# Performance work log

Hardware: AMD Instinct MI355X
Metric: run time of the kernel (lower is better)

## Reference

```python
import jax, jax.numpy as jnp
import numpy as np

N_HEADS = 16
D_MODEL = 1024
D_K = 64
D_V = 64
LN_EPS = 1e-6


def setup_inputs() -> dict:
    key = jax.random.key(0)
    ks = jax.random.split(key, 16)
    B, L, D = 4, 512, D_MODEL
    s = 1.0 / np.sqrt(D)
    return {
        "q": jax.random.normal(ks[0], (B, L, D), jnp.float32),
        "k": jax.random.normal(ks[1], (B, L, D), jnp.float32),
        "v": jax.random.normal(ks[2], (B, L, D), jnp.float32),
        "bias": jax.random.normal(ks[3], (B, N_HEADS, L, L), jnp.float32),
        "graph_attn_bias": jax.random.normal(ks[4], (B, N_HEADS, L, L), jnp.float32),
        # projection weights stored as [in, out] (math-equivalent to torch Linear)
        "wq": jax.random.normal(ks[5], (D, N_HEADS * D_K), jnp.float32) * s,
        "bq": jnp.zeros((N_HEADS * D_K,), jnp.float32),
        "wk": jax.random.normal(ks[6], (D, N_HEADS * D_K), jnp.float32) * s,
        "bk": jnp.zeros((N_HEADS * D_K,), jnp.float32),
        "wv": jax.random.normal(ks[7], (D, N_HEADS * D_V), jnp.float32) * s,
        "bv": jnp.zeros((N_HEADS * D_V,), jnp.float32),
        "wo": jax.random.normal(ks[8], (N_HEADS * D_V, D), jnp.float32) * s,
        "bo": jnp.zeros((D,), jnp.float32),
        "ln_g": jnp.ones((D,), jnp.float32),
        "ln_b": jnp.zeros((D,), jnp.float32),
    }


def reference(q, k, v, bias, graph_attn_bias, wq, bq, wk, bk, wv, bv, wo, bo, ln_g, ln_b):
    B, Lq, D = q.shape
    H, dk, dv = N_HEADS, D_K, D_V
    residual = q
    # fused QKV projections, split heads -> [B, H, L, d]
    qh = (q @ wq + bq).reshape(B, Lq, H, dk).transpose(0, 2, 1, 3)
    kh = (k @ wk + bk).reshape(B, k.shape[1], H, dk).transpose(0, 2, 1, 3)
    vh = (v @ wv + bv).reshape(B, v.shape[1], H, dv).transpose(0, 2, 1, 3)
    # graph scaled dot-product attention: scores + mask bias + structural bias
    scores = jnp.einsum("bhqd,bhkd->bhqk", qh / np.sqrt(dk).astype(qh.dtype), kh)
    scores = scores + bias + graph_attn_bias
    weights = jax.nn.softmax(scores, axis=-1)
    ctx = jnp.einsum("bhqk,bhkd->bhqd", weights, vh)  # [B,H,Lq,dv]
    ctx = ctx.transpose(0, 2, 1, 3).reshape(B, Lq, H * dv)
    out = ctx @ wo + bo + residual
    # LayerNorm(eps=1e-6)
    mu = jnp.mean(out, axis=-1, keepdims=True)
    var = jnp.var(out, axis=-1, keepdims=True)
    out = (out - mu) * jax.lax.rsqrt(var + LN_EPS) * ln_g + ln_b
    return out
```

## Files before the change

kernel.cpp:

```cpp
#include <hip/hip_runtime.h>

#define D_MODEL 1024
#define N_HEADS 16
#define DK 64
#define LSEQ 512
#define BATCH 4
#define M_ROWS (BATCH * LSEQ)

typedef unsigned short ushort_t;
typedef __attribute__((ext_vector_type(8))) short short8;
typedef __attribute__((ext_vector_type(4))) float floatx4;

__device__ __forceinline__ float bf2f(unsigned short u) {
    return __uint_as_float(((unsigned int)u) << 16);
}
__device__ __forceinline__ unsigned short f2bf(float f) {
    unsigned int u = __float_as_uint(f);
    u += 0x7fffu + ((u >> 16) & 1u);
    return (unsigned short)(u >> 16);
}

__global__ __launch_bounds__(256) void cast3_kernel(
    const float* __restrict__ a, const float* __restrict__ b,
    const float* __restrict__ c, ushort_t* __restrict__ oa,
    ushort_t* __restrict__ ob, ushort_t* __restrict__ oc, int n)
{
    const float* src = (blockIdx.y == 0) ? a : (blockIdx.y == 1) ? b : c;
    ushort_t* dst = (blockIdx.y == 0) ? oa : (blockIdx.y == 1) ? ob : oc;
    int i = (blockIdx.x * 256 + threadIdx.x) * 4;
    if (i + 3 < n) {
        float4 v = *(const float4*)(src + i);
        ushort4 o = make_ushort4(f2bf(v.x), f2bf(v.y), f2bf(v.z), f2bf(v.w));
        *(ushort4*)(dst + i) = o;
    }
}

__global__ __launch_bounds__(256) void transpose4_kernel(
    const float* __restrict__ w0, const float* __restrict__ w1,
    const float* __restrict__ w2, const float* __restrict__ w3,
    ushort_t* __restrict__ o0, ushort_t* __restrict__ o1,
    ushort_t* __restrict__ o2, ushort_t* __restrict__ o3)
{
    __shared__ float tile[32][33];
    const float* W = (blockIdx.z == 0) ? w0 : (blockIdx.z == 1) ? w1
                   : (blockIdx.z == 2) ? w2 : w3;
    ushort_t* O = (blockIdx.z == 0) ? o0 : (blockIdx.z == 1) ? o1
                : (blockIdx.z == 2) ? o2 : o3;
    const int tx = threadIdx.x & 31;
    const int ty = threadIdx.x >> 5;
    const int kbase = blockIdx.y * 32;
    const int nbase = blockIdx.x * 32;
    #pragma unroll
    for (int j = 0; j < 4; ++j)
        tile[ty + 8 * j][tx] = W[(size_t)(kbase + ty + 8 * j) * 1024 + nbase + tx];
    __syncthreads();
    #pragma unroll
    for (int j = 0; j < 4; ++j) {
        int n = nbase + ty + 8 * j;
        O[(size_t)n * 1024 + kbase + tx] = f2bf(tile[tx][ty + 8 * j]);
    }
}

template <bool OUT_BF16, bool ADD_RES>
__device__ __forceinline__ void gemm_bt_body(
    const ushort_t* __restrict__ A, const ushort_t* __restrict__ Bt,
    const float* __restrict__ bvec, const float* __restrict__ res,
    void* __restrict__ outp, int M, int N, int K,
    int rowBase, int colBase, ushort_t* As, ushort_t* Bs)
{
    const int tid = threadIdx.x;
    const int l = tid & 63;
    const int w = tid >> 6;
    const int wave_m = w >> 1;
    const int wave_n = w & 1;

    const int srow = l >> 2;
    const int skof = (l & 3) * 8;
    const ushort_t* gA = A  + (size_t)(rowBase + w * 16 + srow) * K + skof;
    const ushort_t* gB = Bt + (size_t)(colBase + w * 16 + srow) * K + skof;
    ushort_t* lA = As + w * 512;
    ushort_t* lB = Bs + w * 512;

    floatx4 acc[2][2];
    #pragma unroll
    for (int i = 0; i < 2; ++i)
        #pragma unroll
        for (int j = 0; j < 2; ++j)
            acc[i][j] = (floatx4){0.f, 0.f, 0.f, 0.f};

    const int fm = l & 15;
    const int fk = (l >> 4) * 8;

    for (int k0 = 0; k0 < K; k0 += 32) {
        __builtin_amdgcn_global_load_lds(
            (const __attribute__((address_space(1))) void*)(gA + k0),
            (__attribute__((address_space(3))) void*)lA, 16, 0, 0);
        __builtin_amdgcn_global_load_lds(
            (const __attribute__((address_space(1))) void*)(gB + k0),
            (__attribute__((address_space(3))) void*)lB, 16, 0, 0);
        __syncthreads();

        short8 afrag[2], bfrag[2];
        #pragma unroll
        for (int mi = 0; mi < 2; ++mi)
            afrag[mi] = *(const short8*)&As[(wave_m * 32 + mi * 16 + fm) * 32 + fk];
        #pragma unroll
        for (int ni = 0; ni < 2; ++ni)
            bfrag[ni] = *(const short8*)&Bs[(wave_n * 32 + ni * 16 + fm) * 32 + fk];

        #pragma unroll
        for (int mi = 0; mi < 2; ++mi)
            #pragma unroll
            for (int ni = 0; ni < 2; ++ni)
                acc[mi][ni] = __builtin_amdgcn_mfma_f32_16x16x32_bf16(
                    afrag[mi], bfrag[ni], acc[mi][ni], 0, 0, 0);
        __syncthreads();
    }

    const int crow0 = rowBase + wave_m * 32 + (l >> 4) * 4;
    const int ccol0 = colBase + wave_n * 32 + (l & 15);
    #pragma unroll
    for (int mi = 0; mi < 2; ++mi) {
        #pragma unroll
        for (int ni = 0; ni < 2; ++ni) {
            const int col = ccol0 + ni * 16;
            const float bb = bvec[col];
            #pragma unroll
            for (int r = 0; r < 4; ++r) {
                const int row = crow0 + mi * 16 + r;
                float v = acc[mi][ni][r] + bb;
                if (ADD_RES) v += res[(size_t)row * N + col];
                if (OUT_BF16)
                    ((ushort_t*)outp)[(size_t)row * N + col] = f2bf(v);
                else
                    ((float*)outp)[(size_t)row * N + col] = v;
            }
        }
    }
}

__global__ __launch_bounds__(256) void gemm_qkv(
    const ushort_t* a0, const ushort_t* a1, const ushort_t* a2,
    const ushort_t* t0, const ushort_t* t1, const ushort_t* t2,
    const float* b0, const float* b1, const float* b2,
    ushort_t* o0, ushort_t* o1, ushort_t* o2)
{
    __shared__ ushort_t As[64 * 32];
    __shared__ ushort_t Bs[64 * 32];
    const int z = blockIdx.z;
    const ushort_t* A  = (z == 0) ? a0 : (z == 1) ? a1 : a2;
    const ushort_t* Bt = (z == 0) ? t0 : (z == 1) ? t1 : t2;
    const float* bv    = (z == 0) ? b0 : (z == 1) ? b1 : b2;
    ushort_t* o        = (z == 0) ? o0 : (z == 1) ? o1 : o2;
    gemm_bt_body<true, false>(A, Bt, bv, nullptr, o, M_ROWS, D_MODEL, D_MODEL,
                              blockIdx.y * 64, blockIdx.x * 64, As, Bs);
}

__global__ __launch_bounds__(256) void gemm_out(
    const ushort_t* __restrict__ A, const ushort_t* __restrict__ Bt,
    const float* __restrict__ bvec, const float* __restrict__ res,
    float* __restrict__ outp)
{
    __shared__ ushort_t As[64 * 32];
    __shared__ ushort_t Bs[64 * 32];
    gemm_bt_body<false, true>(A, Bt, bvec, res, outp, M_ROWS, D_MODEL, D_MODEL,
                              blockIdx.y * 64, blockIdx.x * 64, As, Bs);
}

__global__ __launch_bounds__(256) void attn_mfma(
    const ushort_t* __restrict__ qh, const ushort_t* __restrict__ kh,
    const ushort_t* __restrict__ vh, const float* __restrict__ bias,
    const float* __restrict__ gbias, ushort_t* __restrict__ ctx)
{
    __shared__ ushort_t Qs[16 * 72];
    __shared__ float S[16 * 516];
    __shared__ float Vt[64 * 36];
    __shared__ float red[16][17];
    __shared__ float rowmax[16];
    __shared__ float rowinv[16];

    const int tid = threadIdx.x;
    const int l = tid & 63;
    const int w = tid >> 6;
    const int m = l & 15;
    const int g = l >> 4;

    const int bh = blockIdx.y;
    const int h = bh & (N_HEADS - 1);
    const int b = bh >> 4;
    const int q0 = blockIdx.x * 16;

    const ushort_t* Qg = qh + ((size_t)(b * LSEQ + q0)) * D_MODEL + h * DK;
    const ushort_t* Kg = kh + ((size_t)(b * LSEQ)) * D_MODEL + h * DK;
    const ushort_t* Vg = vh + ((size_t)(b * LSEQ)) * D_MODEL + h * DK;
    const float* biasp  = bias  + ((size_t)bh * LSEQ + q0) * LSEQ;
    const float* gbiasp = gbias + ((size_t)bh * LSEQ + q0) * LSEQ;

    if (tid < 128) {
        int row = tid >> 3, seg = tid & 7;
        short8 t = *(const short8*)(Qg + (size_t)row * D_MODEL + seg * 8);
        *(short8*)&Qs[row * 72 + seg * 8] = t;
    }
    __syncthreads();

    short8 aq0 = *(const short8*)&Qs[m * 72 + g * 8];
    short8 aq1 = *(const short8*)&Qs[m * 72 + g * 8 + 32];

    #pragma unroll 2
    for (int it = 0; it < 8; ++it) {
        const int kb = it * 64 + w * 16;
        const ushort_t* kr = Kg + (size_t)(kb + m) * D_MODEL + g * 8;
        short8 bk0 = *(const short8*)kr;
        short8 bk1 = *(const short8*)(kr + 32);
        floatx4 acc = (floatx4){0.f, 0.f, 0.f, 0.f};
        acc = __builtin_amdgcn_mfma_f32_16x16x32_bf16(aq0, bk0, acc, 0, 0, 0);
        acc = __builtin_amdgcn_mfma_f32_16x16x32_bf16(aq1, bk1, acc, 0, 0, 0);
        const int col = kb + m;
        const int qrow0 = g * 4;
        const float* bp = biasp  + (size_t)qrow0 * LSEQ + col;
        const float* gp = gbiasp + (size_t)qrow0 * LSEQ + col;
        #pragma unroll
        for (int r = 0; r < 4; ++r) {
            float v = acc[r] * 0.125f + bp[(size_t)r * LSEQ] + gp[(size_t)r * LSEQ];
            S[(qrow0 + r) * 516 + col] = v;
        }
    }
    __syncthreads();

    {
        const int row = tid >> 4, sc = tid & 15;
        float* Srow = &S[row * 516];
        float mx = -1e30f;
        #pragma unroll
        for (int i = 0; i < 16; ++i) {
            float2 v = *(float2*)&Srow[2 * sc + 32 * i];
            mx = fmaxf(mx, fmaxf(v.x, v.y));
        }
        red[row][sc] = mx;
        __syncthreads();
        if (tid < 16) {
            float mm = red[tid][0];
            #pragma unroll
            for (int c = 1; c < 16; ++c) mm = fmaxf(mm, red[tid][c]);
            rowmax[tid] = mm;
        }
        __syncthreads();
        mx = rowmax[row];
        float sum = 0.f;
        unsigned pk[16];
        #pragma unroll
        for (int i = 0; i < 16; ++i) {
            float2 v = *(float2*)&Srow[2 * sc + 32 * i];
            float e0 = __expf(v.x - mx);
            float e1 = __expf(v.y - mx);
            sum += e0 + e1;
            pk[i] = (unsigned)f2bf(e0) | ((unsigned)f2bf(e1) << 16);
        }
        red[row][sc] = sum;
        __syncthreads();
        if (tid < 16) {
            float t = 0.f;
            #pragma unroll
            for (int c = 0; c < 16; ++c) t += red[tid][c];
            rowinv[tid] = 1.0f / t;
        }
        unsigned* Pd = (unsigned*)Srow;
        #pragma unroll
        for (int i = 0; i < 16; ++i)
            Pd[sc + 16 * i] = pk[i];
    }

    const ushort_t* Ps = (const ushort_t*)S;
    floatx4 oacc = (floatx4){0.f, 0.f, 0.f, 0.f};
    const unsigned* VtD = (const unsigned*)Vt;

    for (int vt = 0; vt < 8; ++vt) {
        const int kv0 = vt * 64;
        __syncthreads();
        {
            const int kp = tid & 31, dg = tid >> 5;
            const ushort_t* vr = Vg + (size_t)(kv0 + 2 * kp) * D_MODEL + dg * 8;
            short8 r0 = *(const short8*)vr;
            short8 r1 = *(const short8*)(vr + D_MODEL);
            unsigned* vtp = (unsigned*)Vt;
            #pragma unroll
            for (int i = 0; i < 8; ++i) {
                unsigned dwv = (unsigned)(ushort_t)r0[i]
                             | ((unsigned)(ushort_t)r1[i] << 16);
                vtp[(dg * 8 + i) * 36 + kp] = dwv;
            }
        }
        __syncthreads();
        #pragma unroll
        for (int kt = 0; kt < 2; ++kt) {
            short8 pf = *(const short8*)&Ps[(size_t)m * 1032 + kv0 + kt * 32 + g * 8];
            short8 vf = *(const short8*)&VtD[(w * 16 + m) * 36 + kt * 16 + g * 4];
            oacc = __builtin_amdgcn_mfma_f32_16x16x32_bf16(pf, vf, oacc, 0, 0, 0);
        }
    }

    {
        const int qrow0 = g * 4;
        const int dcol = w * 16 + m;
        ushort_t* cp = ctx + ((size_t)(b * LSEQ + q0 + qrow0)) * D_MODEL + h * DK + dcol;
        #pragma unroll
        for (int r = 0; r < 4; ++r)
            cp[(size_t)r * D_MODEL] = f2bf(oacc[r] * rowinv[qrow0 + r]);
    }
}

__global__ __launch_bounds__(256) void ln_kernel(
    float* __restrict__ x, const float* __restrict__ g,
    const float* __restrict__ beta)
{
    const int row = blockIdx.x;
    float* xr = x + (size_t)row * D_MODEL;
    const int tid = threadIdx.x;

    float v[4];
    float s = 0.f, sq = 0.f;
    #pragma unroll
    for (int j = 0; j < 4; ++j) {
        v[j] = xr[tid + 256 * j];
        s += v[j];
        sq += v[j] * v[j];
    }
    __shared__ float rs[256], rq[256];
    rs[tid] = s;
    rq[tid] = sq;
    __syncthreads();
    for (int st = 128; st > 0; st >>= 1) {
        if (tid < st) { rs[tid] += rs[tid + st]; rq[tid] += rq[tid + st]; }
        __syncthreads();
    }
    const float mean = rs[0] * (1.0f / D_MODEL);
    const float var = rq[0] * (1.0f / D_MODEL) - mean * mean;
    const float rinv = rsqrtf(var + 1e-6f);
    #pragma unroll
    for (int j = 0; j < 4; ++j) {
        int n = tid + 256 * j;
        xr[n] = (v[j] - mean) * rinv * g[n] + beta[n];
    }
}

extern "C" void kernel_launch(void* const* d_in, const int* in_sizes, int n_in,
                              void* d_out, int out_size, void* d_ws, size_t ws_size,
                              hipStream_t stream)
{
    const float* q     = (const float*)d_in[0];
    const float* k     = (const float*)d_in[1];
    const float* v     = (const float*)d_in[2];
    const float* bias  = (const float*)d_in[3];
    const float* gbias = (const float*)d_in[4];
    const float* wq    = (const float*)d_in[5];
    const float* bq    = (const float*)d_in[6];
    const float* wk    = (const float*)d_in[7];
    const float* bk    = (const float*)d_in[8];
    const float* wv    = (const float*)d_in[9];
    const float* bv    = (const float*)d_in[10];
    const float* wo    = (const float*)d_in[11];
    const float* bo    = (const float*)d_in[12];
    const float* ln_g  = (const float*)d_in[13];
    const float* ln_b  = (const float*)d_in[14];

    const size_t MB = 1u << 20;
    char* wsb = (char*)d_ws;
    ushort_t* vb   = (ushort_t*)(wsb + 0 * MB);
    ushort_t* wqb  = (ushort_t*)(wsb + 4 * MB);
    ushort_t* wkb  = (ushort_t*)(wsb + 6 * MB);
    ushort_t* wvb  = (ushort_t*)(wsb + 8 * MB);
    ushort_t* wob  = (ushort_t*)(wsb + 10 * MB);
    ushort_t* qhb  = (ushort_t*)(wsb + 12 * MB);
    ushort_t* khb  = (ushort_t*)(wsb + 16 * MB);
    ushort_t* vhb  = (ushort_t*)(wsb + 20 * MB);
    ushort_t* ctxb = (ushort_t*)(wsb + 24 * MB);
    ushort_t* qb = (ushort_t*)d_out;
    ushort_t* kb = (ushort_t*)d_out + (size_t)M_ROWS * D_MODEL;
    float* outp = (float*)d_out;

    const int NELEM = M_ROWS * D_MODEL;

    cast3_kernel<<<dim3(NELEM / 1024, 3), 256, 0, stream>>>(
        q, k, v, qb, kb, vb, NELEM);
    transpose4_kernel<<<dim3(32, 32, 4), 256, 0, stream>>>(
        wq, wk, wv, wo, wqb, wkb, wvb, wob);

    dim3 gqkv(D_MODEL / 64, M_ROWS / 64, 3);
    gemm_qkv<<<gqkv, 256, 0, stream>>>(
        qb, kb, vb, wqb, wkb, wvb, bq, bk, bv, qhb, khb, vhb);

    dim3 ablk(LSEQ / 16, BATCH * N_HEADS);
    attn_mfma<<<ablk, 256, 0, stream>>>(qhb, khb, vhb, bias, gbias, ctxb);

    dim3 gout(D_MODEL / 64, M_ROWS / 64);
    gemm_out<<<gout, 256, 0, stream>>>(ctxb, wob, bo, q, outp);

    ln_kernel<<<M_ROWS, 256, 0, stream>>>(outp, ln_g, ln_b);
}
```

Baseline: 277.9 us.

## Widen GEMM K-tile with swizzled LDS, split-K out-projection, vectorize attention bias loads

The GEMM body now stages 64-wide K tiles through LDS with an XOR-style column rotation, which halves the number of barriers per K and is meant to avoid LDS bank conflicts. The output projection is split into two K halves across blockIdx.z, doubling the grid; the second partial is written to a workspace buffer that LayerNorm adds back in. In attention, the bias and graph-bias reads move from scattered per-MFMA-lane scalar loads into coalesced float4 loads in the softmax pass. Costs are extra traffic for the partial output buffer and higher register use from holding the scores.

```diff
diff --git a/kernel.cpp b/kernel.cpp
--- a/kernel.cpp
+++ b/kernel.cpp
@@ -61,11 +61,11 @@
     }
 }
 
-template <bool OUT_BF16, bool ADD_RES>
+template <bool OUT_BF16, bool ADD_BVEC, bool ADD_RES>
 __device__ __forceinline__ void gemm_bt_body(
     const ushort_t* __restrict__ A, const ushort_t* __restrict__ Bt,
     const float* __restrict__ bvec, const float* __restrict__ res,
-    void* __restrict__ outp, int M, int N, int K,
+    void* __restrict__ outp, int N, int K, int kStart, int kEnd,
     int rowBase, int colBase, ushort_t* As, ushort_t* Bs)
 {
     const int tid = threadIdx.x;
@@ -74,12 +74,16 @@
     const int wave_m = w >> 1;
     const int wave_n = w & 1;
 
-    const int srow = l >> 2;
-    const int skof = (l & 3) * 8;
-    const ushort_t* gA = A  + (size_t)(rowBase + w * 16 + srow) * K + skof;
-    const ushort_t* gB = Bt + (size_t)(colBase + w * 16 + srow) * K + skof;
-    ushort_t* lA = As + w * 512;
-    ushort_t* lB = Bs + w * 512;
+    const int srow8 = l >> 3;
+    const int cgl = ((l & 7) + srow8) & 7;
+    const ushort_t* gA0 = A  + (size_t)(rowBase + w * 16 + 0 + srow8) * K + cgl * 8;
+    const ushort_t* gA1 = A  + (size_t)(rowBase + w * 16 + 8 + srow8) * K + cgl * 8;
+    const ushort_t* gB0 = Bt + (size_t)(colBase + w * 16 + 0 + srow8) * K + cgl * 8;
+    const ushort_t* gB1 = Bt + (size_t)(colBase + w * 16 + 8 + srow8) * K + cgl * 8;
+    ushort_t* lA0 = As + w * 1024;
+    ushort_t* lA1 = As + w * 1024 + 512;
+    ushort_t* lB0 = Bs + w * 1024;
+    ushort_t* lB1 = Bs + w * 1024 + 512;
 
     floatx4 acc[2][2];
     #pragma unroll
@@ -89,42 +93,60 @@
             acc[i][j] = (floatx4){0.f, 0.f, 0.f, 0.f};
 
     const int fm = l & 15;
-    const int fk = (l >> 4) * 8;
-
-    for (int k0 = 0; k0 < K; k0 += 32) {
+    const int fg = l >> 4;
+
+    for (int k0 = kStart; k0 < kEnd; k0 += 64) {
         __builtin_amdgcn_global_load_lds(
-            (const __attribute__((address_space(1))) void*)(gA + k0),
-            (__attribute__((address_space(3))) void*)lA, 16, 0, 0);
+            (const __attribute__((address_space(1))) void*)(gA0 + k0),
+            (__attribute__((address_space(3))) void*)lA0, 16, 0, 0);
         __builtin_amdgcn_global_load_lds(
-            (const __attribute__((address_space(1))) void*)(gB + k0),
-            (__attribute__((address_space(3))) void*)lB, 16, 0, 0);
-        __syncthreads();
-
-        short8 afrag[2], bfrag[2];
+            (const __attribute__((address_space(1))) void*)(gA1 + k0),
+            (__attribute__((address_space(3))) void*)lA1, 16, 0, 0);
+        __builtin_amdgcn_global_load_lds(
+            (const __attribute__((address_space(1))) void*)(gB0 + k0),
+            (__attribute__((address_space(3))) void*)lB0, 16, 0, 0);
+        __builtin_amdgcn_global_load_lds(
+            (const __attribute__((address_space(1))) void*)(gB1 + k0),
+            (__attribute__((address_space(3))) void*)lB1, 16, 0, 0);
+        __syncthreads();
+
+        short8 afrag[2][2], bfrag[2][2];
         #pragma unroll
         for (int mi = 0; mi < 2; ++mi)
-            afrag[mi] = *(const short8*)&As[(wave_m * 32 + mi * 16 + fm) * 32 + fk];
+            #pragma unroll
+            for (int kt = 0; kt < 2; ++kt) {
+                int p = ((kt * 4 + fg) - fm) & 7;
+                afrag[mi][kt] = *(const short8*)
+                    &As[(wave_m * 32 + mi * 16 + fm) * 64 + p * 8];
+            }
         #pragma unroll
         for (int ni = 0; ni < 2; ++ni)
-            bfrag[ni] = *(const short8*)&Bs[(wave_n * 32 + ni * 16 + fm) * 32 + fk];
-
-        #pragma unroll
-        for (int mi = 0; mi < 2; ++mi)
-            #pragma unroll
-            for (int ni = 0; ni < 2; ++ni)
-                acc[mi][ni] = __builtin_amdgcn_mfma_f32_16x16x32_bf16(
-                    afrag[mi], bfrag[ni], acc[mi][ni], 0, 0, 0);
-        __syncthreads();
-    }
-
-    const int crow0 = rowBase + wave_m * 32 + (l >> 4) * 4;
-    const int ccol0 = colBase + wave_n * 32 + (l & 15);
+            #pragma unroll
+            for (int kt = 0; kt < 2; ++kt) {
+                int p = ((kt * 4 + fg) - fm) & 7;
+                bfrag[ni][kt] = *(const short8*)
+                    &Bs[(wave_n * 32 + ni * 16 + fm) * 64 + p * 8];
+            }
+
+        #pragma unroll
+        for (int kt = 0; kt < 2; ++kt)
+            #pragma unroll
+            for (int mi = 0; mi < 2; ++mi)
+                #pragma unroll
+                for (int ni = 0; ni < 2; ++ni)
+                    acc[mi][ni] = __builtin_amdgcn_mfma_f32_16x16x32_bf16(
+                        afrag[mi][kt], bfrag[ni][kt], acc[mi][ni], 0, 0, 0);
+        __syncthreads();
+    }
+
+    const int crow0 = rowBase + wave_m * 32 + fg * 4;
+    const int ccol0 = colBase + wave_n * 32 + fm;
     #pragma unroll
     for (int mi = 0; mi < 2; ++mi) {
         #pragma unroll
         for (int ni = 0; ni < 2; ++ni) {
             const int col = ccol0 + ni * 16;
-            const float bb = bvec[col];
+            const float bb = ADD_BVEC ? bvec[col] : 0.f;
             #pragma unroll
             for (int r = 0; r < 4; ++r) {
                 const int row = crow0 + mi * 16 + r;
@@ -145,26 +167,33 @@
     const float* b0, const float* b1, const float* b2,
     ushort_t* o0, ushort_t* o1, ushort_t* o2)
 {
-    __shared__ ushort_t As[64 * 32];
-    __shared__ ushort_t Bs[64 * 32];
+    __shared__ ushort_t As[64 * 64];
+    __shared__ ushort_t Bs[64 * 64];
     const int z = blockIdx.z;
     const ushort_t* A  = (z == 0) ? a0 : (z == 1) ? a1 : a2;
     const ushort_t* Bt = (z == 0) ? t0 : (z == 1) ? t1 : t2;
     const float* bv    = (z == 0) ? b0 : (z == 1) ? b1 : b2;
     ushort_t* o        = (z == 0) ? o0 : (z == 1) ? o1 : o2;
-    gemm_bt_body<true, false>(A, Bt, bv, nullptr, o, M_ROWS, D_MODEL, D_MODEL,
-                              blockIdx.y * 64, blockIdx.x * 64, As, Bs);
+    gemm_bt_body<true, true, false>(A, Bt, bv, nullptr, o, D_MODEL, D_MODEL,
+                                    0, D_MODEL,
+                                    blockIdx.y * 64, blockIdx.x * 64, As, Bs);
 }
 
 __global__ __launch_bounds__(256) void gemm_out(
     const ushort_t* __restrict__ A, const ushort_t* __restrict__ Bt,
     const float* __restrict__ bvec, const float* __restrict__ res,
-    float* __restrict__ outp)
-{
-    __shared__ ushort_t As[64 * 32];
-    __shared__ ushort_t Bs[64 * 32];
-    gemm_bt_body<false, true>(A, Bt, bvec, res, outp, M_ROWS, D_MODEL, D_MODEL,
-                              blockIdx.y * 64, blockIdx.x * 64, As, Bs);
+    float* __restrict__ out0, float* __restrict__ out1)
+{
+    __shared__ ushort_t As[64 * 64];
+    __shared__ ushort_t Bs[64 * 64];
+    if (blockIdx.z == 0)
+        gemm_bt_body<false, true, true>(A, Bt, bvec, res, out0, D_MODEL,
+                                        D_MODEL, 0, 512,
+                                        blockIdx.y * 64, blockIdx.x * 64, As, Bs);
+    else
+        gemm_bt_body<false, false, false>(A, Bt, nullptr, nullptr, out1, D_MODEL,
+                                          D_MODEL, 512, 1024,
+                                          blockIdx.y * 64, blockIdx.x * 64, As, Bs);
 }
 
 __global__ __launch_bounds__(256) void attn_mfma(
@@ -193,8 +222,6 @@
     const ushort_t* Qg = qh + ((size_t)(b * LSEQ + q0)) * D_MODEL + h * DK;
     const ushort_t* Kg = kh + ((size_t)(b * LSEQ)) * D_MODEL + h * DK;
     const ushort_t* Vg = vh + ((size_t)(b * LSEQ)) * D_MODEL + h * DK;
-    const float* biasp  = bias  + ((size_t)bh * LSEQ + q0) * LSEQ;
-    const float* gbiasp = gbias + ((size_t)bh * LSEQ + q0) * LSEQ;
 
     if (tid < 128) {
         int row = tid >> 3, seg = tid & 7;
@@ -217,26 +244,32 @@
         acc = __builtin_amdgcn_mfma_f32_16x16x32_bf16(aq1, bk1, acc, 0, 0, 0);
         const int col = kb + m;
         const int qrow0 = g * 4;
-        const float* bp = biasp  + (size_t)qrow0 * LSEQ + col;
-        const float* gp = gbiasp + (size_t)qrow0 * LSEQ + col;
-        #pragma unroll
-        for (int r = 0; r < 4; ++r) {
-            float v = acc[r] * 0.125f + bp[(size_t)r * LSEQ] + gp[(size_t)r * LSEQ];
-            S[(qrow0 + r) * 516 + col] = v;
-        }
+        #pragma unroll
+        for (int r = 0; r < 4; ++r)
+            S[(qrow0 + r) * 516 + col] = acc[r] * 0.125f;
     }
     __syncthreads();
 
     {
-        const int row = tid >> 4, sc = tid & 15;
+        const int row = tid >> 4, s = tid & 15;
         float* Srow = &S[row * 516];
+        const float* bp = bias  + ((size_t)bh * LSEQ + q0 + row) * LSEQ;
+        const float* gp = gbias + ((size_t)bh * LSEQ + q0 + row) * LSEQ;
+
+        float4 vv[8];
         float mx = -1e30f;
         #pragma unroll
-        for (int i = 0; i < 16; ++i) {
-            float2 v = *(float2*)&Srow[2 * sc + 32 * i];
-            mx = fmaxf(mx, fmaxf(v.x, v.y));
-        }
-        red[row][sc] = mx;
+        for (int i = 0; i < 8; ++i) {
+            const int col = 4 * s + 64 * i;
+            float4 sv = *(const float4*)&Srow[col];
+            float4 bb = *(const float4*)(bp + col);
+            float4 gg = *(const float4*)(gp + col);
+            float4 v = make_float4(sv.x + bb.x + gg.x, sv.y + bb.y + gg.y,
+                                   sv.z + bb.z + gg.z, sv.w + bb.w + gg.w);
+            vv[i] = v;
+            mx = fmaxf(mx, fmaxf(fmaxf(v.x, v.y), fmaxf(v.z, v.w)));
+        }
+        red[row][s] = mx;
         __syncthreads();
         if (tid < 16) {
             float mm = red[tid][0];
@@ -246,17 +279,20 @@
         }
         __syncthreads();
         mx = rowmax[row];
+
         float sum = 0.f;
-        unsigned pk[16];
-        #pragma unroll
-        for (int i = 0; i < 16; ++i) {
-            float2 v = *(float2*)&Srow[2 * sc + 32 * i];
-            float e0 = __expf(v.x - mx);
-            float e1 = __expf(v.y - mx);
-            sum += e0 + e1;
-            pk[i] = (unsigned)f2bf(e0) | ((unsigned)f2bf(e1) << 16);
-        }
-        red[row][sc] = sum;
+        unsigned* Pd = (unsigned*)Srow;
+        #pragma unroll
+        for (int i = 0; i < 8; ++i) {
+            float e0 = __expf(vv[i].x - mx);
+            float e1 = __expf(vv[i].y - mx);
+            float e2 = __expf(vv[i].z - mx);
+            float e3 = __expf(vv[i].w - mx);
+            sum += (e0 + e1) + (e2 + e3);
+            Pd[2 * s + 32 * i]     = (unsigned)f2bf(e0) | ((unsigned)f2bf(e1) << 16);
+            Pd[2 * s + 32 * i + 1] = (unsigned)f2bf(e2) | ((unsigned)f2bf(e3) << 16);
+        }
+        red[row][s] = sum;
         __syncthreads();
         if (tid < 16) {
             float t = 0.f;
@@ -264,10 +300,6 @@
             for (int c = 0; c < 16; ++c) t += red[tid][c];
             rowinv[tid] = 1.0f / t;
         }
-        unsigned* Pd = (unsigned*)Srow;
-        #pragma unroll
-        for (int i = 0; i < 16; ++i)
-            Pd[sc + 16 * i] = pk[i];
     }
 
     const ushort_t* Ps = (const ushort_t*)S;
@@ -310,18 +342,19 @@
 }
 
 __global__ __launch_bounds__(256) void ln_kernel(
-    float* __restrict__ x, const float* __restrict__ g,
-    const float* __restrict__ beta)
+    float* __restrict__ x, const float* __restrict__ part2,
+    const float* __restrict__ g, const float* __restrict__ beta)
 {
     const int row = blockIdx.x;
     float* xr = x + (size_t)row * D_MODEL;
+    const float* pr = part2 + (size_t)row * D_MODEL;
     const int tid = threadIdx.x;
 
     float v[4];
     float s = 0.f, sq = 0.f;
     #pragma unroll
     for (int j = 0; j < 4; ++j) {
-        v[j] = xr[tid + 256 * j];
+        v[j] = xr[tid + 256 * j] + pr[tid + 256 * j];
         s += v[j];
         sq += v[j] * v[j];
     }
@@ -374,6 +407,7 @@
     ushort_t* khb  = (ushort_t*)(wsb + 16 * MB);
     ushort_t* vhb  = (ushort_t*)(wsb + 20 * MB);
     ushort_t* ctxb = (ushort_t*)(wsb + 24 * MB);
+    float* out1 = (float*)(wsb + 12 * MB);
     ushort_t* qb = (ushort_t*)d_out;
     ushort_t* kb = (ushort_t*)d_out + (size_t)M_ROWS * D_MODEL;
     float* outp = (float*)d_out;
@@ -392,8 +426,8 @@
     dim3 ablk(LSEQ / 16, BATCH * N_HEADS);
     attn_mfma<<<ablk, 256, 0, stream>>>(qhb, khb, vhb, bias, gbias, ctxb);
 
-    dim3 gout(D_MODEL / 64, M_ROWS / 64);
-    gemm_out<<<gout, 256, 0, stream>>>(ctxb, wob, bo, q, outp);
-
-    ln_kernel<<<M_ROWS, 256, 0, stream>>>(outp, ln_g, ln_b);
-}
+    dim3 gout(D_MODEL / 64, M_ROWS / 64, 2);
+    gemm_out<<<gout, 256, 0, stream>>>(ctxb, wob, bo, q, outp, out1);
+
+    ln_kernel<<<M_ROWS, 256, 0, stream>>>(outp, out1, ln_g, ln_b);
+}
```

New measurement: 272.0 us. -2.1%, faster.
